# Optimization experiments

Hardware: AMD Instinct MI355X
Metric: run time of the kernel (lower is better)

Reference implementation:

```python
import jax, jax.numpy as jnp
import numpy as np

B, S, H = 32, 2048, 1024

def setup_inputs() -> dict:
    key = jax.random.key(0)
    k1, k2, k3, k4, k5 = jax.random.split(key, 5)
    hidden = jax.random.normal(k1, (1, B, H), dtype=jnp.float32)
    encoder_outputs = jax.random.normal(k2, (B, S, H), dtype=jnp.float32)
    # nn.Linear(2H, H): weight [H, 2H], bias [H]
    W_attn = jax.random.normal(k3, (H, 2 * H), dtype=jnp.float32) * (1.0 / np.sqrt(2 * H))
    b_attn = jax.random.normal(k4, (H,), dtype=jnp.float32) * 0.01
    # nn.Linear(H, 1, bias=False): weight [1, H] -> stored as [H]
    v = jax.random.normal(k5, (H,), dtype=jnp.float32) * (1.0 / np.sqrt(H))
    return {"hidden": hidden, "encoder_outputs": encoder_outputs,
            "W_attn": W_attn, "b_attn": b_attn, "v": v}

def reference(hidden, encoder_outputs, W_attn, b_attn, v):
    # hidden: [1, B, H] -> [B, H]; encoder_outputs: [B, S, H]
    h = hidden[0]  # [B, H]
    # cat((hidden_repeated, enc), -1) @ W_attn.T == h @ Wh.T + enc @ We.T
    Wh = W_attn[:, :H]   # [H, H] acts on hidden part
    We = W_attn[:, H:]   # [H, H] acts on encoder part
    h_proj = jnp.einsum('bh,oh->bo', h, Wh)                    # [B, H]
    e_proj = jnp.einsum('bsh,oh->bso', encoder_outputs, We)    # [B, S, H]
    energy = jnp.tanh(e_proj + h_proj[:, None, :] + b_attn)    # [B, S, H]
    attention = jnp.einsum('bsh,h->bs', energy, v)             # [B, S]
    return jax.nn.softmax(attention, axis=1)
```

## Files before the change

### kernel.cpp

```cpp
#include <hip/hip_runtime.h>
#include <hip/hip_bf16.h>
#include <cstdint>


#define HDIM 1024
#define SDIM 2048
#define MTOT 65536

typedef __attribute__((ext_vector_type(8))) short short8;
typedef __attribute__((ext_vector_type(4))) float floatx4;

__device__ __forceinline__ unsigned short f2bf(float f) {
    unsigned int u = __float_as_uint(f);
    u += 0x7fffu + ((u >> 16) & 1u);
    return (unsigned short)(u >> 16);
}
__device__ __forceinline__ unsigned int pack2(float a, float b) {
    return (unsigned int)f2bf(a) | ((unsigned int)f2bf(b) << 16);
}
__device__ __forceinline__ float fast_tanh(float x) {
    float e2 = __expf(2.f * x);
    return 1.f - 2.f * __builtin_amdgcn_rcpf(e2 + 1.f);
}

__global__ __launch_bounds__(256) void prep(const float* __restrict__ W,
                                            unsigned short* __restrict__ Wbf2,
                                            const float* __restrict__ hid,
                                            const float* __restrict__ bias,
                                            float* __restrict__ c) {
    __shared__ float red[4][32];
    if (blockIdx.x < 512) {
        int T = blockIdx.x * 256 + threadIdx.x;
        int n  = T >> 7;
        int k8 = T & 127;
        int k  = k8 * 8;
        const float4* src = (const float4*)(W + (size_t)n * 2048 + 1024 + k);
        float4 f0 = src[0], f1 = src[1];
        int jt = n >> 4, lc = n & 15, kc = k8 >> 2, g = k8 & 3;
        uint4 u;
        u.x = pack2(f0.x, f0.y); u.y = pack2(f0.z, f0.w);
        u.z = pack2(f1.x, f1.y); u.w = pack2(f1.z, f1.w);
        *(uint4*)(Wbf2 + (size_t)(jt * 32 + kc) * 512 + (g * 16 + lc) * 8) = u;
    } else {
        const int o = blockIdx.x - 512;
        const int wave = threadIdx.x >> 6, lane = threadIdx.x & 63;
        const int k = wave * 256 + lane * 4;
        const float4 wv = *(const float4*)(W + (size_t)o * 2048 + k);
        float acc[32];
#pragma unroll
        for (int b = 0; b < 32; ++b) {
            const float4 h = *(const float4*)(hid + b * HDIM + k);
            acc[b] = wv.x * h.x + wv.y * h.y + wv.z * h.z + wv.w * h.w;
        }
#pragma unroll
        for (int b = 0; b < 32; ++b) {
            float x = acc[b];
            for (int off = 32; off; off >>= 1) x += __shfl_xor(x, off);
            if (lane == 0) red[wave][b] = x;
        }
        __syncthreads();
        if (threadIdx.x < 32) {
            int b = threadIdx.x;
            c[b * HDIM + o] = red[0][b] + red[1][b] + red[2][b] + red[3][b] + bias[o];
        }
    }
}

#define PHN 8
#define PHK 128

__global__ __launch_bounds__(512, 2) void attn_fused(const float* __restrict__ enc,
                                                     const unsigned short* __restrict__ Wbf2,
                                                     const float* __restrict__ c,
                                                     const float* __restrict__ v,
                                                     float* __restrict__ logits) {
    __shared__ __align__(16) unsigned short slab[2][64 * 128];

    const int tid  = threadIdx.x;
    const int lane = tid & 63;
    const int wave = tid >> 6;
    const int grp  = lane >> 4;
    const int lc   = lane & 15;

    const int m0 = blockIdx.x * 64;
    const int b  = m0 >> 11;

    const int s_kk   = (lane & 31) * 4;
    const int s_rsub = lane >> 5;
    const int s_c16  = (lane & 31) >> 1;
    const int s_b8   = lane & 1;

    floatx4 acc[2][4][4];
#pragma unroll
    for (int cg = 0; cg < 2; ++cg)
#pragma unroll
        for (int i = 0; i < 4; ++i)
#pragma unroll
            for (int j = 0; j < 4; ++j) acc[cg][i][j] = (floatx4){0.f, 0.f, 0.f, 0.f};

    const short8* Bfr = (const short8*)Wbf2;

    float4 ld[4];
#pragma unroll
    for (int q = 0; q < 4; ++q) {
        int row = wave * 8 + q * 2 + s_rsub;
        ld[q] = *(const float4*)(enc + (size_t)(m0 + row) * HDIM + s_kk);
    }
#pragma unroll
    for (int q = 0; q < 4; ++q) {
        int row  = wave * 8 + q * 2 + s_rsub;
        int slot = s_c16 ^ (row & 7);
        uint2 u = {pack2(ld[q].x, ld[q].y), pack2(ld[q].z, ld[q].w)};
        *(uint2*)(&slab[0][row * 128 + slot * 8 + s_b8 * 4]) = u;
    }

    short8 bf[4], bn[4];
#pragma unroll
    for (int j = 0; j < 4; ++j)
        bf[j] = Bfr[(size_t)((wave * 8 + 0 * 4 + j) * 32 + 0) * 64 + lane];

#pragma unroll 1
    for (int p = 0; p < PHN; ++p) {
        __syncthreads();

        if (p < PHN - 1) {
#pragma unroll
            for (int q = 0; q < 4; ++q) {
                int row = wave * 8 + q * 2 + s_rsub;
                ld[q] = *(const float4*)(enc + (size_t)(m0 + row) * HDIM +
                                         (p + 1) * PHK + s_kk);
            }
        }

        const unsigned short* sl = slab[p & 1];
#pragma unroll
        for (int s = 0; s < 8; ++s) {
            const int cg = s >> 2, kc = s & 3;
            short8 af[4];
#pragma unroll
            for (int i = 0; i < 4; ++i) {
                int row  = i * 16 + lc;
                int slot = (kc * 4 + grp) ^ (lc & 7);
                af[i] = *(const short8*)(sl + row * 128 + slot * 16 / 2);
            }
            {
                const int cg2 = (s < 7) ? ((s + 1) >> 2) : 0;
                const int kc2 = (s < 7) ? ((s + 1) & 3) : 0;
                const int pn  = (s < 7) ? p : ((p < PHN - 1) ? p + 1 : p);
#pragma unroll
                for (int j = 0; j < 4; ++j)
                    bn[j] = Bfr[(size_t)((wave * 8 + cg2 * 4 + j) * 32 +
                                         pn * 4 + kc2) * 64 + lane];
            }
            __builtin_amdgcn_s_setprio(1);
#pragma unroll
            for (int i = 0; i < 4; ++i)
#pragma unroll
                for (int j = 0; j < 4; ++j)
                    acc[cg][i][j] = __builtin_amdgcn_mfma_f32_16x16x32_bf16(
                        af[i], bf[j], acc[cg][i][j], 0, 0, 0);
            __builtin_amdgcn_s_setprio(0);
            if (p < PHN - 1 && s >= 4) {
                const int q = s - 4;
                int row  = wave * 8 + q * 2 + s_rsub;
                int slot = s_c16 ^ (row & 7);
                uint2 u = {pack2(ld[q].x, ld[q].y), pack2(ld[q].z, ld[q].w)};
                *(uint2*)(&slab[(p + 1) & 1][row * 128 + slot * 8 + s_b8 * 4]) = u;
            }
#pragma unroll
            for (int j = 0; j < 4; ++j) bf[j] = bn[j];
        }
    }

    float rowsum[4][4];
#pragma unroll
    for (int i = 0; i < 4; ++i)
#pragma unroll
        for (int r = 0; r < 4; ++r) rowsum[i][r] = 0.f;

#pragma unroll
    for (int cg = 0; cg < 2; ++cg)
#pragma unroll
        for (int j = 0; j < 4; ++j) {
            const int n  = wave * 128 + cg * 64 + j * 16 + lc;
            const float vn = v[n];
            const float cv = c[b * HDIM + n];
#pragma unroll
            for (int i = 0; i < 4; ++i)
#pragma unroll
                for (int r = 0; r < 4; ++r)
                    rowsum[i][r] = fmaf(fast_tanh(acc[cg][i][j][r] + cv), vn,
                                        rowsum[i][r]);
        }

    float* red = (float*)slab;
#pragma unroll
    for (int i = 0; i < 4; ++i)
#pragma unroll
        for (int r = 0; r < 4; ++r) {
            float x = rowsum[i][r];
            x += __shfl_xor(x, 8);
            x += __shfl_xor(x, 4);
            x += __shfl_xor(x, 2);
            x += __shfl_xor(x, 1);
            if (lc == 0) red[wave * 64 + i * 16 + grp * 4 + r] = x;
        }
    __syncthreads();
    if (tid < 64) {
        float ssum = 0.f;
#pragma unroll
        for (int w = 0; w < 8; ++w) ssum += red[w * 64 + tid];
        logits[m0 + tid] = ssum;
    }
}

__global__ __launch_bounds__(256) void softmax_k(const float* __restrict__ logits,
                                                 float* __restrict__ out) {
    __shared__ float wred[4];
    const int bb = blockIdx.x;
    const int tid = threadIdx.x;
    const int wave = tid >> 6, lane = tid & 63;

    float vals[8];
    float lmax = -INFINITY;
#pragma unroll
    for (int q = 0; q < 8; ++q) {
        vals[q] = logits[(size_t)bb * SDIM + q * 256 + tid];
        lmax = fmaxf(lmax, vals[q]);
    }
    for (int off = 32; off; off >>= 1) lmax = fmaxf(lmax, __shfl_xor(lmax, off));
    if (lane == 0) wred[wave] = lmax;
    __syncthreads();
    lmax = fmaxf(fmaxf(wred[0], wred[1]), fmaxf(wred[2], wred[3]));
    __syncthreads();

    float e[8];
    float s = 0.f;
#pragma unroll
    for (int q = 0; q < 8; ++q) {
        e[q] = __expf(vals[q] - lmax);
        s += e[q];
    }
    for (int off = 32; off; off >>= 1) s += __shfl_xor(s, off);
    if (lane == 0) wred[wave] = s;
    __syncthreads();
    s = wred[0] + wred[1] + wred[2] + wred[3];
    const float inv = 1.f / s;
#pragma unroll
    for (int q = 0; q < 8; ++q)
        out[(size_t)bb * SDIM + q * 256 + tid] = e[q] * inv;
}

extern "C" void kernel_launch(void* const* d_in, const int* in_sizes, int n_in,
                              void* d_out, int out_size, void* d_ws, size_t ws_size,
                              hipStream_t stream) {
    const float* hidden = (const float*)d_in[0];
    const float* enc    = (const float*)d_in[1];
    const float* W      = (const float*)d_in[2];
    const float* battn  = (const float*)d_in[3];
    const float* v      = (const float*)d_in[4];
    float* out = (float*)d_out;

    char* ws = (char*)d_ws;
    float* c             = (float*)ws;
    float* logits        = (float*)(ws + (128 << 10));
    unsigned short* Wbf2 = (unsigned short*)(ws + (384 << 10));

    hipLaunchKernelGGL(prep,       dim3(1536), dim3(256), 0, stream, W, Wbf2, hidden, battn, c);
    hipLaunchKernelGGL(attn_fused, dim3(1024), dim3(512), 0, stream, enc, Wbf2, c, v, logits);
    hipLaunchKernelGGL(softmax_k,  dim3(32),   dim3(256), 0, stream, logits, out);
}
```

Baseline: 521.7 us.

## Retile fused attention GEMM to 128-row strips split across two N-halves

Each block now covers 128 encoder rows and half of the output columns instead of 64 rows and all columns. Two blocks per strip write separate partial logits, and the softmax kernel adds them. This raises reuse of each W fragment across more rows per wave. In exchange, every encoder row is loaded and converted to bf16 twice, and LDS use doubles to 64KB. The LDS writes for the next phase are also moved after the MFMA loop rather than interleaved with it, and the setprio hints are dropped.

```diff
diff --git a/kernel.cpp b/kernel.cpp
--- a/kernel.cpp
+++ b/kernel.cpp
@@ -73,8 +73,8 @@
                                                      const unsigned short* __restrict__ Wbf2,
                                                      const float* __restrict__ c,
                                                      const float* __restrict__ v,
-                                                     float* __restrict__ logits) {
-    __shared__ __align__(16) unsigned short slab[2][64 * 128];
+                                                     float* __restrict__ part) {
+    __shared__ __align__(16) unsigned short slab[2][128 * 128];
 
     const int tid  = threadIdx.x;
     const int lane = tid & 63;
@@ -82,33 +82,35 @@
     const int grp  = lane >> 4;
     const int lc   = lane & 15;
 
-    const int m0 = blockIdx.x * 64;
+    const int strip = blockIdx.x >> 1;
+    const int nhalf = blockIdx.x & 1;
+    const int m0 = strip * 128;
     const int b  = m0 >> 11;
+    const int cb = nhalf * 512 + wave * 64;
 
     const int s_kk   = (lane & 31) * 4;
     const int s_rsub = lane >> 5;
     const int s_c16  = (lane & 31) >> 1;
     const int s_b8   = lane & 1;
 
-    floatx4 acc[2][4][4];
-#pragma unroll
-    for (int cg = 0; cg < 2; ++cg)
-#pragma unroll
-        for (int i = 0; i < 4; ++i)
-#pragma unroll
-            for (int j = 0; j < 4; ++j) acc[cg][i][j] = (floatx4){0.f, 0.f, 0.f, 0.f};
+    floatx4 acc[8][4];
+#pragma unroll
+    for (int i = 0; i < 8; ++i)
+#pragma unroll
+        for (int j = 0; j < 4; ++j) acc[i][j] = (floatx4){0.f, 0.f, 0.f, 0.f};
 
     const short8* Bfr = (const short8*)Wbf2;
-
-    float4 ld[4];
-#pragma unroll
-    for (int q = 0; q < 4; ++q) {
-        int row = wave * 8 + q * 2 + s_rsub;
+    const int jt0 = nhalf * 32 + wave * 4;
+
+    float4 ld[8];
+#pragma unroll
+    for (int q = 0; q < 8; ++q) {
+        int row = wave * 16 + q * 2 + s_rsub;
         ld[q] = *(const float4*)(enc + (size_t)(m0 + row) * HDIM + s_kk);
     }
 #pragma unroll
-    for (int q = 0; q < 4; ++q) {
-        int row  = wave * 8 + q * 2 + s_rsub;
+    for (int q = 0; q < 8; ++q) {
+        int row  = wave * 16 + q * 2 + s_rsub;
         int slot = s_c16 ^ (row & 7);
         uint2 u = {pack2(ld[q].x, ld[q].y), pack2(ld[q].z, ld[q].w)};
         *(uint2*)(&slab[0][row * 128 + slot * 8 + s_b8 * 4]) = u;
@@ -117,7 +119,7 @@
     short8 bf[4], bn[4];
 #pragma unroll
     for (int j = 0; j < 4; ++j)
-        bf[j] = Bfr[(size_t)((wave * 8 + 0 * 4 + j) * 32 + 0) * 64 + lane];
+        bf[j] = Bfr[(size_t)((jt0 + j) * 32 + 0) * 64 + lane];
 
 #pragma unroll 1
     for (int p = 0; p < PHN; ++p) {
@@ -125,8 +127,8 @@
 
         if (p < PHN - 1) {
 #pragma unroll
-            for (int q = 0; q < 4; ++q) {
-                int row = wave * 8 + q * 2 + s_rsub;
+            for (int q = 0; q < 8; ++q) {
+                int row = wave * 16 + q * 2 + s_rsub;
                 ld[q] = *(const float4*)(enc + (size_t)(m0 + row) * HDIM +
                                          (p + 1) * PHK + s_kk);
             }
@@ -134,68 +136,66 @@
 
         const unsigned short* sl = slab[p & 1];
 #pragma unroll
-        for (int s = 0; s < 8; ++s) {
-            const int cg = s >> 2, kc = s & 3;
-            short8 af[4];
-#pragma unroll
-            for (int i = 0; i < 4; ++i) {
+        for (int s = 0; s < 4; ++s) {
+            const int kc = s;
+            short8 af[8];
+#pragma unroll
+            for (int i = 0; i < 8; ++i) {
                 int row  = i * 16 + lc;
                 int slot = (kc * 4 + grp) ^ (lc & 7);
-                af[i] = *(const short8*)(sl + row * 128 + slot * 16 / 2);
+                af[i] = *(const short8*)(sl + row * 128 + slot * 8);
             }
             {
-                const int cg2 = (s < 7) ? ((s + 1) >> 2) : 0;
-                const int kc2 = (s < 7) ? ((s + 1) & 3) : 0;
-                const int pn  = (s < 7) ? p : ((p < PHN - 1) ? p + 1 : p);
+                const int kc2 = (s + 1) & 3;
+                const int pn  = (s < 3) ? p : ((p < PHN - 1) ? p + 1 : p);
 #pragma unroll
                 for (int j = 0; j < 4; ++j)
-                    bn[j] = Bfr[(size_t)((wave * 8 + cg2 * 4 + j) * 32 +
-                                         pn * 4 + kc2) * 64 + lane];
-            }
-            __builtin_amdgcn_s_setprio(1);
-#pragma unroll
-            for (int i = 0; i < 4; ++i)
+                    bn[j] = Bfr[(size_t)((jt0 + j) * 32 + pn * 4 + kc2) * 64 + lane];
+            }
+#pragma unroll
+            for (int i = 0; i < 8; ++i)
 #pragma unroll
                 for (int j = 0; j < 4; ++j)
-                    acc[cg][i][j] = __builtin_amdgcn_mfma_f32_16x16x32_bf16(
-                        af[i], bf[j], acc[cg][i][j], 0, 0, 0);
-            __builtin_amdgcn_s_setprio(0);
-            if (p < PHN - 1 && s >= 4) {
-                const int q = s - 4;
-                int row  = wave * 8 + q * 2 + s_rsub;
+                    acc[i][j] = __builtin_amdgcn_mfma_f32_16x16x32_bf16(
+                        af[i], bf[j], acc[i][j], 0, 0, 0);
+#pragma unroll
+            for (int j = 0; j < 4; ++j) bf[j] = bn[j];
+        }
+
+        if (p < PHN - 1) {
+#pragma unroll
+            for (int q = 0; q < 8; ++q) {
+                int row  = wave * 16 + q * 2 + s_rsub;
                 int slot = s_c16 ^ (row & 7);
                 uint2 u = {pack2(ld[q].x, ld[q].y), pack2(ld[q].z, ld[q].w)};
                 *(uint2*)(&slab[(p + 1) & 1][row * 128 + slot * 8 + s_b8 * 4]) = u;
             }
-#pragma unroll
-            for (int j = 0; j < 4; ++j) bf[j] = bn[j];
-        }
-    }
-
-    float rowsum[4][4];
-#pragma unroll
-    for (int i = 0; i < 4; ++i)
+        }
+    }
+
+    float rowsum[8][4];
+#pragma unroll
+    for (int i = 0; i < 8; ++i)
 #pragma unroll
         for (int r = 0; r < 4; ++r) rowsum[i][r] = 0.f;
 
 #pragma unroll
-    for (int cg = 0; cg < 2; ++cg)
-#pragma unroll
-        for (int j = 0; j < 4; ++j) {
-            const int n  = wave * 128 + cg * 64 + j * 16 + lc;
-            const float vn = v[n];
-            const float cv = c[b * HDIM + n];
-#pragma unroll
-            for (int i = 0; i < 4; ++i)
-#pragma unroll
-                for (int r = 0; r < 4; ++r)
-                    rowsum[i][r] = fmaf(fast_tanh(acc[cg][i][j][r] + cv), vn,
-                                        rowsum[i][r]);
-        }
-
+    for (int j = 0; j < 4; ++j) {
+        const int n  = cb + j * 16 + lc;
+        const float vn = v[n];
+        const float cv = c[b * HDIM + n];
+#pragma unroll
+        for (int i = 0; i < 8; ++i)
+#pragma unroll
+            for (int r = 0; r < 4; ++r)
+                rowsum[i][r] = fmaf(fast_tanh(acc[i][j][r] + cv), vn,
+                                    rowsum[i][r]);
+    }
+
+    __syncthreads();
     float* red = (float*)slab;
 #pragma unroll
-    for (int i = 0; i < 4; ++i)
+    for (int i = 0; i < 8; ++i)
 #pragma unroll
         for (int r = 0; r < 4; ++r) {
             float x = rowsum[i][r];
@@ -203,18 +203,18 @@
             x += __shfl_xor(x, 4);
             x += __shfl_xor(x, 2);
             x += __shfl_xor(x, 1);
-            if (lc == 0) red[wave * 64 + i * 16 + grp * 4 + r] = x;
-        }
-    __syncthreads();
-    if (tid < 64) {
+            if (lc == 0) red[wave * 128 + i * 16 + grp * 4 + r] = x;
+        }
+    __syncthreads();
+    if (tid < 128) {
         float ssum = 0.f;
 #pragma unroll
-        for (int w = 0; w < 8; ++w) ssum += red[w * 64 + tid];
-        logits[m0 + tid] = ssum;
-    }
-}
-
-__global__ __launch_bounds__(256) void softmax_k(const float* __restrict__ logits,
+        for (int w = 0; w < 8; ++w) ssum += red[w * 128 + tid];
+        part[(size_t)nhalf * MTOT + m0 + tid] = ssum;
+    }
+}
+
+__global__ __launch_bounds__(256) void softmax_k(const float* __restrict__ part,
                                                  float* __restrict__ out) {
     __shared__ float wred[4];
     const int bb = blockIdx.x;
@@ -225,7 +225,8 @@
     float lmax = -INFINITY;
 #pragma unroll
     for (int q = 0; q < 8; ++q) {
-        vals[q] = logits[(size_t)bb * SDIM + q * 256 + tid];
+        const size_t idx = (size_t)bb * SDIM + q * 256 + tid;
+        vals[q] = part[idx] + part[(size_t)MTOT + idx];
         lmax = fmaxf(lmax, vals[q]);
     }
     for (int off = 32; off; off >>= 1) lmax = fmaxf(lmax, __shfl_xor(lmax, off));
@@ -263,10 +264,10 @@
 
     char* ws = (char*)d_ws;
     float* c             = (float*)ws;
-    float* logits        = (float*)(ws + (128 << 10));
-    unsigned short* Wbf2 = (unsigned short*)(ws + (384 << 10));
+    float* part          = (float*)(ws + (128 << 10));
+    unsigned short* Wbf2 = (unsigned short*)(ws + (640 << 10));
 
     hipLaunchKernelGGL(prep,       dim3(1536), dim3(256), 0, stream, W, Wbf2, hidden, battn, c);
-    hipLaunchKernelGGL(attn_fused, dim3(1024), dim3(512), 0, stream, enc, Wbf2, c, v, logits);
-    hipLaunchKernelGGL(softmax_k,  dim3(32),   dim3(256), 0, stream, logits, out);
-}
+    hipLaunchKernelGGL(attn_fused, dim3(1024), dim3(512), 0, stream, enc, Wbf2, c, v, part);
+    hipLaunchKernelGGL(softmax_k,  dim3(32),   dim3(256), 0, stream, part, out);
+}
```

Result: faster. 491.9 us (-5.7%).
